# Performance work log

Hardware: AMD Instinct MI355X
Metric: run time of the kernel (lower is better)

The kernel has to match this reference:

```python
import jax, jax.numpy as jnp
import numpy as np
jax.config.update("jax_enable_x64", True)

K = 10            # num_digits
NUM_CLASSES = 10  # digit classes 0..9
EQ_TOKEN = 28
PRIMES = np.array([7, 11, 13, 17, 19, 23, 29, 31, 37], dtype=np.int64)
TWO_PI = 2.0 * np.pi
M_TOTAL = int(np.prod(PRIMES.astype(object)))  # product of primes ~2.47e11 (needs int64)
_crt = []
for p in PRIMES:
    Mi = M_TOTAL // int(p)
    _crt.append((Mi * pow(Mi, -1, int(p))) % M_TOTAL)
CRT_C = jnp.array(_crt, dtype=jnp.int64)                 # [P] CRT mixing coefficients
POW10 = jnp.array([[pow(10, k, int(p)) for k in range(K)] for p in PRIMES], dtype=jnp.float32)  # [P,K]
PR_F = jnp.array(PRIMES, dtype=jnp.float32)
PR_I = jnp.array(PRIMES, dtype=jnp.int64)
POW10_DEC = jnp.array([10 ** k for k in range(K)], dtype=jnp.int64)
_op = np.full(64, -1, dtype=np.int64)
_op[20:25] = np.arange(5)  # tokens 20..24 -> ops add,sub,mul,exp,div
OP_TABLE = jnp.array(_op)


def encode(d):
    # d [B,S,K] soft base-10 digits -> RNS circle encoding [B,S,P,2]
    theta = TWO_PI * jnp.einsum('bsk,pk->bsp', d, POW10) / PR_F
    return jnp.stack([jnp.cos(theta), jnp.sin(theta)], axis=-1)


def decode_residues(circle):
    # [B,S,P,2] -> integer residues mod p, [B,S,P] int64
    theta = jnp.arctan2(circle[..., 1], circle[..., 0])
    r = jnp.round(theta / TWO_PI * PR_F).astype(jnp.int64)
    return jnp.mod(r, PR_I)


def circle_add(a, b):
    ca, sa = a[..., 0], a[..., 1]
    cb, sb = b[..., 0], b[..., 1]
    return jnp.stack([ca * cb - sa * sb, sa * cb + ca * sb], axis=-1)


def circle_sub(a, b):
    ca, sa = a[..., 0], a[..., 1]
    cb, sb = b[..., 0], b[..., 1]
    return jnp.stack([ca * cb + sa * sb, sa * cb - ca * sb], axis=-1)


def modpow(base, exp, mod):
    # elementwise modular exponentiation, exponents < 64 (6 square-and-multiply steps)
    res = jnp.ones_like(base)
    b = jnp.mod(base, mod)
    e = exp
    for _ in range(6):
        res = jnp.where((e & 1) == 1, (res * b) % mod, res)
        b = (b * b) % mod
        e = e >> 1
    return res


def crt(residues):
    # CRT reconstruction: [B,S,P] -> [B,S] int64 in [0, M_TOTAL)
    return jnp.mod(jnp.sum(residues * CRT_C, axis=-1), M_TOTAL)


def crt_signed(residues):
    n = crt(residues)
    return jnp.where(n > M_TOTAL // 2, n - M_TOTAL, n)


def int_to_digits(n):
    # [B,S] int64 -> [B,S,K] float base-10 digits, LSB-first
    return ((n[..., None] // POW10_DEC) % 10).astype(jnp.float32)


def int_to_digits_signed(n):
    sign = (n < 0).astype(jnp.float32)[..., None]
    return jnp.concatenate([int_to_digits(jnp.abs(n)), sign], axis=-1)  # [B,S,K+1]


def decode_all_ops(a_c, b_c):
    # All 5 operations decoded to digit vectors -> [B,S,5K+1]
    ra = decode_residues(a_c)
    rb = decode_residues(b_c)
    add_d = int_to_digits(crt(decode_residues(circle_add(a_c, b_c))))
    sub_d = int_to_digits_signed(crt_signed(decode_residues(circle_sub(a_c, b_c))))
    mul_d = int_to_digits(crt((ra * rb) % PR_I))
    exp_d = int_to_digits(crt(modpow(ra, rb, PR_I)))
    inv = modpow(rb, PR_I - 2, PR_I)  # Fermat inverse
    div_r = jnp.where(rb == 0, 0, (ra * inv) % PR_I)
    div_d = int_to_digits(crt(div_r))
    return jnp.concatenate([add_d, sub_d, mul_d, exp_d, div_d], axis=-1)


def select_op(results, input_ids):
    # [B,S,5K+1] -> [B,S,K+1]: pick the relevant operation per sequence
    B, S, _ = results.shape
    pad = jnp.zeros((B, S, 1), results.dtype)
    ops = jnp.stack([
        jnp.concatenate([results[..., 0:K], pad], -1),
        results[..., K:2 * K + 1],
        jnp.concatenate([results[..., 2 * K + 1:3 * K + 1], pad], -1),
        jnp.concatenate([results[..., 3 * K + 1:4 * K + 1], pad], -1),
        jnp.concatenate([results[..., 4 * K + 1:5 * K + 1], pad], -1),
    ], axis=-2)  # [B,S,5,K+1]
    is_op = OP_TABLE[jnp.clip(input_ids, 0, 63)] >= 0
    op_pos = jnp.argmax(is_op, axis=1)  # first operator position per sequence
    op_tok = jnp.take_along_axis(input_ids, op_pos[:, None], axis=1)[:, 0]
    op_idx = OP_TABLE[jnp.clip(op_tok, 0, 63)]
    gidx = jnp.broadcast_to(jnp.clip(op_idx, 0, 4)[:, None, None, None], (B, S, 1, K + 1))
    sel = jnp.take_along_axis(ops, gidx, axis=-2)[..., 0, :]
    valid = (op_idx >= 0).astype(results.dtype)[:, None, None]
    return sel * valid


def reorder_msb(res):
    # LSB-first digits -> MSB-first, -1 sentinel past the last significant digit
    digits = res[..., :K]
    sign = res[..., K:]
    idx = jnp.arange(K)
    nz = digits != 0
    highest = jnp.max(jnp.where(nz, idx, -1), axis=-1)
    num_sig = jnp.where(jnp.any(nz, axis=-1), highest + 1, 1)
    src = jnp.clip(num_sig[..., None] - 1 - idx, 0, K - 1)
    msb = jnp.take_along_axis(digits, src, axis=-1)
    msb = jnp.where(idx < num_sig[..., None], msb, -1.0)
    return jnp.concatenate([msb, sign], axis=-1)


def setup_inputs() -> dict:
    key = jax.random.key(0)
    ks = jax.random.split(key, 6)
    B, S, D, MH = 16, 2048, 768, 128
    h = jax.random.normal(ks[0], (B, S, D), dtype=jnp.float32)
    input_ids = jax.random.randint(ks[1], (B, S), 0, 50, dtype=jnp.int64)
    W1 = jax.random.normal(ks[2], (D, MH), dtype=jnp.float32) * 0.02
    b1 = jnp.zeros((MH,), jnp.float32)
    W2 = jax.random.normal(ks[3], (MH, 2 * K * NUM_CLASSES), dtype=jnp.float32) * 0.02
    b2 = jnp.zeros((2 * K * NUM_CLASSES,), jnp.float32)
    Winj = jax.random.normal(ks[4], (K + 1, D), dtype=jnp.float32) * 0.001  # injector_init_std
    binj = jnp.zeros((D,), jnp.float32)
    gate_logit = jnp.array(-2.0, jnp.float32)  # gate_init_logit
    return {"h": h, "W1": W1, "b1": b1, "W2": W2, "b2": b2,
            "Winj": Winj, "binj": binj, "gate_logit": gate_logit, "input_ids": input_ids}


def reference(h, W1, b1, W2, b2, Winj, binj, gate_logit, input_ids):
    B, S, D = h.shape
    # OperandExtractor: per-token MLP -> soft digits for operands a and b
    hid = jax.nn.relu(h @ W1 + b1)
    logits = (hid @ W2 + b2).reshape(B, S, 2, K, NUM_CLASSES)
    probs = jax.nn.softmax(logits, axis=-1)
    dig = jnp.einsum('bsokc,c->bsok', probs, jnp.arange(NUM_CLASSES, dtype=h.dtype))
    d_a, d_b = dig[..., 0, :], dig[..., 1, :]
    # RNSCircleEncoder (frozen)
    a_c = encode(d_a)
    b_c = encode(d_b)
    # ArithmeticCompute + CRT decode: detached (torch.no_grad in original)
    results = jax.lax.stop_gradient(decode_all_ops(a_c, b_c).astype(h.dtype))
    sel = select_op(results, input_ids)
    msb = reorder_msb(sel)
    # ResultInjector: gated linear injection into the residual stream
    inj = msb @ Winj + binj
    h_prime = h + jax.nn.sigmoid(gate_logit) * inj
    # only inject for sequences containing the '=' token
    has_eq = jnp.any(input_ids == EQ_TOKEN, axis=1).astype(h.dtype)[:, None, None]
    h_prime = h + (h_prime - h) * has_eq
    return h_prime, d_a, d_b
```

## Files before the change

### kernel.cpp

```cpp
#include <hip/hip_runtime.h>

typedef unsigned short u16;
typedef unsigned int   u32;
typedef unsigned long long u64;
typedef long long i64;

typedef __attribute__((ext_vector_type(8))) short short8;
typedef __attribute__((ext_vector_type(4))) float f32x4;

#define DEV static __device__ __forceinline__

__constant__ float POW10F[9][10] = {
  {1,3,2,6,4,5,1,3,2,6},
  {1,10,1,10,1,10,1,10,1,10},
  {1,10,9,12,3,4,1,10,9,12},
  {1,10,15,14,4,6,9,5,16,7},
  {1,10,5,12,6,3,11,15,17,18},
  {1,10,8,11,18,19,6,14,2,20},
  {1,10,13,14,24,8,22,17,25,18},
  {1,10,7,8,18,25,2,20,14,16},
  {1,10,26,1,10,26,1,10,26,1},
};

#define M_TOTAL  247357937827ull
#define M_HALF   123678968913ull

DEV u16 f2bf_rne(float f){
  u32 u = __float_as_uint(f);
  return (u16)((u + 0x7FFFu + ((u >> 16) & 1u)) >> 16);
}
DEV float bf2f(u16 v){ return __uint_as_float(((u32)v) << 16); }

DEV short8 pack_bf16(float4 a, float4 b){
  union { short8 s; u32 u[4]; } r;
  r.u[0] = (__float_as_uint(a.x) >> 16) | (__float_as_uint(a.y) & 0xFFFF0000u);
  r.u[1] = (__float_as_uint(a.z) >> 16) | (__float_as_uint(a.w) & 0xFFFF0000u);
  r.u[2] = (__float_as_uint(b.x) >> 16) | (__float_as_uint(b.y) & 0xFFFF0000u);
  r.u[3] = (__float_as_uint(b.z) >> 16) | (__float_as_uint(b.w) & 0xFFFF0000u);
  return r.s;
}

DEV void load_lds16(const void* g, void* l){
  __builtin_amdgcn_global_load_lds((const __attribute__((address_space(1))) void*)g,
                                   (__attribute__((address_space(3))) void*)l, 16, 0, 0);
}

DEV int modpow6(int b, int e, int p){
  int res = 1; b %= p;
  #pragma unroll
  for (int i = 0; i < 6; ++i){
    if (e & 1) res = (res * b) % p;
    b = (b * b) % p;
    e >>= 1;
  }
  return res;
}

__global__ void scan_kernel(const int* __restrict__ ids, int* __restrict__ op_idx,
                            float* __restrict__ has_eq){
  __shared__ int smin[256];
  __shared__ int seq[256];
  int b = blockIdx.x, tid = threadIdx.x;
  int best = 2048, eq = 0;
  for (int i = tid; i < 2048; i += 256){
    int t = ids[b * 2048 + i];
    if (t >= 20 && t < 25) best = min(best, i);
    eq |= (t == 28) ? 1 : 0;
  }
  smin[tid] = best; seq[tid] = eq;
  __syncthreads();
  for (int s = 128; s > 0; s >>= 1){
    if (tid < s){ smin[tid] = min(smin[tid], smin[tid + s]); seq[tid] |= seq[tid + s]; }
    __syncthreads();
  }
  if (tid == 0){
    int op = -1;
    if (smin[0] < 2048) op = ids[b * 2048 + smin[0]] - 20;
    op_idx[b] = op;
    has_eq[b] = seq[0] ? 1.0f : 0.0f;
  }
}

__global__ void prep_kernel(const float* __restrict__ W1, const float* __restrict__ W2,
                            u16* __restrict__ w1f, u16* __restrict__ w2f){
  int tid = blockIdx.x * 256 + threadIdx.x;
  if (tid < 12288){
    int blk = tid >> 6, L = tid & 63;
    int T = blk >> 3, b = blk & 7;
    int q = L >> 4, ln = L & 15;
    #pragma unroll
    for (int j = 0; j < 8; ++j){
      int k = 32 * T + 8 * q + j;
      int n = 16 * b + ln;
      w1f[(size_t)blk * 512 + L * 8 + j] = f2bf_rne(W1[k * 128 + n]);
    }
  } else if (tid < 12288 + 3328){
    int t2 = tid - 12288;
    int blk = t2 >> 6, L = t2 & 63;
    int t = blk / 13, b2 = blk % 13;
    int q = L >> 4, ln = L & 15;
    #pragma unroll
    for (int j = 0; j < 8; ++j){
      int k = 32 * t + 8 * q + j;
      int n = 16 * b2 + ln;
      w2f[(size_t)blk * 512 + L * 8 + j] = (n < 200) ? f2bf_rne(W2[k * 200 + n]) : (u16)0;
    }
  }
}

__launch_bounds__(256, 2)
__global__ void pass1_kernel(const float* __restrict__ h, const u16* __restrict__ w1f,
                             const u16* __restrict__ w2f, const float* __restrict__ b1,
                             const float* __restrict__ b2, const int* __restrict__ op_idx_ws,
                             float* __restrict__ dout, u64* __restrict__ msbp){
  __shared__ u16 w1buf[16384];
  __shared__ u16 hidf[4][2048];
  __shared__ float digits_s[64][20];
  __shared__ float tab_s[64][18];
  __shared__ u64 ops_s[64][5];

  const int tid = threadIdx.x;
  const int w = tid >> 6;
  const int lane = tid & 63;
  const int ln = lane & 15, q = lane >> 4;
  const int wg = blockIdx.x;
  const int tok0 = wg * 64;
  const int gtok = tok0 + w * 16 + ln;

  float b1v[8];
  #pragma unroll
  for (int b = 0; b < 8; ++b) b1v[b] = b1[ln + 16 * b];
  float b2v[13];
  #pragma unroll
  for (int b = 0; b < 13; ++b){ int n = ln + 16 * b; b2v[b] = (n < 200) ? b2[n] : 0.0f; }

  f32x4 acc[8];
  #pragma unroll
  for (int b = 0; b < 8; ++b) acc[b] = (f32x4)0.0f;

  const float* hrow = h + (size_t)gtok * 768;
  for (int c = 0; c < 6; ++c){
    float4 xa[4], xb[4];
    const float4* ap = (const float4*)(hrow + c * 128);
    #pragma unroll
    for (int t = 0; t < 4; ++t){
      xa[t] = ap[t * 8 + q * 2];
      xb[t] = ap[t * 8 + q * 2 + 1];
    }
    __syncthreads();
    #pragma unroll
    for (int i = 0; i < 8; ++i){
      int blk = w * 8 + i;
      load_lds16(w1f + (size_t)(c * 32 + blk) * 512 + lane * 8, &w1buf[blk * 512]);
    }
    __syncthreads();
    short8 af[4];
    #pragma unroll
    for (int t = 0; t < 4; ++t) af[t] = pack_bf16(xa[t], xb[t]);
    #pragma unroll
    for (int t = 0; t < 4; ++t){
      #pragma unroll
      for (int b = 0; b < 8; ++b){
        short8 bf = *(const short8*)&w1buf[(t * 8 + b) * 512 + lane * 8];
        acc[b] = __builtin_amdgcn_mfma_f32_16x16x32_bf16(af[t], bf, acc[b], 0, 0, 0);
      }
    }
  }

  #pragma unroll
  for (int b = 0; b < 8; ++b){
    int t2 = b >> 1;
    int q2 = ((b & 1) << 1) | (ln >> 3);
    int j = ln & 7;
    #pragma unroll
    for (int r = 0; r < 4; ++r){
      float v = acc[b][r] + b1v[b];
      v = fmaxf(v, 0.0f);
      int L2 = (q2 << 4) | (q * 4 + r);
      hidf[w][t2 * 512 + L2 * 8 + j] = (u16)(__float_as_uint(v) >> 16);
    }
  }
  __syncthreads();

  short8 a2[4];
  #pragma unroll
  for (int t = 0; t < 4; ++t) a2[t] = *(const short8*)&hidf[w][t * 512 + lane * 8];
  f32x4 acc2[13];
  #pragma unroll
  for (int b = 0; b < 13; ++b) acc2[b] = (f32x4)0.0f;
  #pragma unroll
  for (int b = 0; b < 13; ++b){
    #pragma unroll
    for (int t = 0; t < 4; ++t){
      short8 bf = *(const short8*)(w2f + (size_t)(t * 13 + b) * 512 + lane * 8);
      acc2[b] = __builtin_amdgcn_mfma_f32_16x16x32_bf16(a2[t], bf, acc2[b], 0, 0, 0);
    }
  }

  __syncthreads();

  #pragma unroll
  for (int b = 0; b < 13; ++b){
    #pragma unroll
    for (int r = 0; r < 4; ++r){
      float v = acc2[b][r] + b2v[b];
      w1buf[w * 4096 + (q * 4 + r) * 212 + ln + 16 * b] = (u16)(__float_as_uint(v) >> 16);
    }
  }
  __syncthreads();

  #pragma unroll
  for (int i = 0; i < 5; ++i){
    int task = tid + i * 256;
    int tok = task / 20, slot = task % 20;
    const u16* lp = &w1buf[(tok >> 4) * 4096 + (tok & 15) * 212 + slot * 10];
    float v[10];
    #pragma unroll
    for (int k = 0; k < 10; ++k) v[k] = bf2f(lp[k]);
    float mx = v[0];
    #pragma unroll
    for (int k = 1; k < 10; ++k) mx = fmaxf(mx, v[k]);
    float s = 0.0f, sd = 0.0f;
    #pragma unroll
    for (int k = 0; k < 10; ++k){
      float e = __expf(v[k] - mx);
      s += e; sd += e * (float)k;
    }
    float dig = sd / s;
    digits_s[tok][slot] = dig;
    int gt = tok0 + tok;
    int o = slot / 10, k10 = slot % 10;
    dout[(size_t)25165824 + (size_t)o * 327680 + (size_t)gt * 10 + k10] = dig;
  }
  __syncthreads();

  #pragma unroll
  for (int i = 0; i < 5; ++i){
    int task = tid + i * 256;
    if (task < 1152){
      int tok = task / 18, rm = task % 18;
      int ab = rm / 9, pi = rm % 9;
      float t = 0.0f;
      #pragma unroll
      for (int k = 0; k < 10; ++k) t += digits_s[tok][ab * 10 + k] * POW10F[pi][k];
      tab_s[tok][ab * 9 + pi] = t;
    }
  }
  __syncthreads();

  {
    constexpr int PR[9] = {7, 11, 13, 17, 19, 23, 29, 31, 37};
    constexpr u64 CRTC[9] = {
      35336848261ull, 224870852570ull, 114165202074ull, 218257003965ull,
      78113032998ull, 53773464745ull, 68236672504ull, 223420072876ull, 220616539143ull
    };
    #pragma unroll
    for (int rep = 0; rep < 2; ++rep){
      int task = tid + rep * 256;
      if (task < 320){
        int op = task >> 6, tok = task & 63;
        u64 acc64 = 0;
        #pragma unroll
        for (int pi = 0; pi < 9; ++pi){
          const int p = PR[pi];
          float ta = tab_s[tok][pi], tb = tab_s[tok][9 + pi];
          int r;
          if (op == 0){
            r = __float2int_rn(ta + tb) % p;
          } else if (op == 1){
            int s = __float2int_rn(ta - tb) % p;
            r = (s < 0) ? s + p : s;
          } else {
            int ra = __float2int_rn(ta) % p;
            int rb = __float2int_rn(tb) % p;
            if (op == 2) r = (ra * rb) % p;
            else if (op == 3) r = modpow6(ra, rb, p);
            else r = (rb == 0) ? 0 : (ra * modpow6(rb, p - 2, p)) % p;
          }
          acc64 += (u64)r * CRTC[pi];
        }
        u64 n = acc64 % M_TOTAL;
        int sign = 0;
        u64 un = n;
        if (op == 1 && n > M_HALF){ sign = 1; un = M_TOTAL - n; }
        u64 pk = 0;
        #pragma unroll
        for (int k = 0; k < 10; ++k){ pk |= (un % 10ull) << (4 * k); un /= 10ull; }
        pk |= ((u64)sign) << 40;
        ops_s[tok][op] = pk;
      }
    }
  }
  __syncthreads();

  if (tid < 64){
    int tok = tid;
    int op = op_idx_ws[wg >> 5];
    u64 pk = (op >= 0) ? ops_s[tok][op] : 0ull;
    int g[10]; int hi = -1;
    #pragma unroll
    for (int k = 0; k < 10; ++k){
      g[k] = (int)((pk >> (4 * k)) & 15ull);
      if (g[k] != 0) hi = k;
    }
    int ns = (hi >= 0) ? hi + 1 : 1;
    u64 mp = 0;
    #pragma unroll
    for (int i = 0; i < 10; ++i){
      int v = (i < ns) ? g[ns - 1 - i] : 15;
      mp |= ((u64)v) << (4 * i);
    }
    mp |= ((pk >> 40) & 1ull) << 40;
    msbp[tok0 + tok] = mp;
  }
}

__launch_bounds__(192)
__global__ void pass2_kernel(const float* __restrict__ h, const float* __restrict__ Winj,
                             const float* __restrict__ binj, const float* __restrict__ gate,
                             const float* __restrict__ has_eq_ws,
                             const u64* __restrict__ msbp, float* __restrict__ dout){
  __shared__ u64 smp[16];
  const int tid = threadIdx.x;
  const int tok0 = blockIdx.x * 16;
  if (tid < 16) smp[tid] = msbp[tok0 + tid];

  float4 wv[11];
  #pragma unroll
  for (int j = 0; j < 11; ++j) wv[j] = *(const float4*)(Winj + (size_t)j * 768 + tid * 4);
  float4 bj = *(const float4*)(binj + tid * 4);
  float G = has_eq_ws[tok0 >> 11] * (1.0f / (1.0f + __expf(-gate[0])));
  __syncthreads();

  #pragma unroll 4
  for (int tt = 0; tt < 16; ++tt){
    u64 mp = smp[tt];
    float v[11];
    #pragma unroll
    for (int k = 0; k < 10; ++k){
      int nib = (int)((mp >> (4 * k)) & 15ull);
      v[k] = (nib == 15) ? -1.0f : (float)nib;
    }
    v[10] = (float)((mp >> 40) & 15ull);
    float ix = bj.x, iy = bj.y, iz = bj.z, iw = bj.w;
    #pragma unroll
    for (int j = 0; j < 11; ++j){
      ix += v[j] * wv[j].x; iy += v[j] * wv[j].y;
      iz += v[j] * wv[j].z; iw += v[j] * wv[j].w;
    }
    size_t off = (size_t)(tok0 + tt) * 768 + tid * 4;
    float4 hv = *(const float4*)(h + off);
    float4 o;
    o.x = hv.x + G * ix; o.y = hv.y + G * iy;
    o.z = hv.z + G * iz; o.w = hv.w + G * iw;
    *(float4*)(dout + off) = o;
  }
}

extern "C" void kernel_launch(void* const* d_in, const int* in_sizes, int n_in,
                              void* d_out, int out_size, void* d_ws, size_t ws_size,
                              hipStream_t stream){
  const float* h    = (const float*)d_in[0];
  const float* W1   = (const float*)d_in[1];
  const float* b1   = (const float*)d_in[2];
  const float* W2   = (const float*)d_in[3];
  const float* b2   = (const float*)d_in[4];
  const float* Winj = (const float*)d_in[5];
  const float* binj = (const float*)d_in[6];
  const float* gate = (const float*)d_in[7];
  const int*   ids  = (const int*)d_in[8];
  float* dout = (float*)d_out;

  char* ws = (char*)d_ws;
  int*   op_idx = (int*)(ws + 0);
  float* has_eq = (float*)(ws + 64);
  u16*   w1f    = (u16*)(ws + 256);
  u16*   w2f    = (u16*)(ws + 256 + 196608);
  u64*   msbp   = (u64*)(ws + 250112);

  scan_kernel<<<16, 256, 0, stream>>>(ids, op_idx, has_eq);
  prep_kernel<<<61, 256, 0, stream>>>(W1, W2, w1f, w2f);
  pass1_kernel<<<512, 256, 0, stream>>>(h, w1f, w2f, b1, b2, op_idx, dout, msbp);
  pass2_kernel<<<2048, 192, 0, stream>>>(h, Winj, binj, gate, has_eq, msbp, dout);
}
```

Baseline: 235.1 us.

## Fuse pass1 and pass2 into one kernel, double-buffer W1 tiles, merge prelude kernels

Merges the token scan and weight-prep kernels into one prelude launch. Fuses the MLP/RNS pass with the injection pass, so the MSB digits stay in LDS instead of going through workspace, and the h rows are reread by the same block, likely while still in cache. The W1 GEMM loop now uses half-size LDS tiles with double buffering, prefetching the next tile and the next h slice during the MFMAs. The trade-offs are fewer launches and less global traffic against larger LDS use, the Winj copy into LDS, and only 192 of 256 threads active in the injection phase.

Result: no change. 234.2 us (-0.4%).

```diff
diff --git a/kernel.cpp b/kernel.cpp
--- a/kernel.cpp
+++ b/kernel.cpp
@@ -3,7 +3,6 @@
 typedef unsigned short u16;
 typedef unsigned int   u32;
 typedef unsigned long long u64;
-typedef long long i64;
 
 typedef __attribute__((ext_vector_type(8))) short short8;
 typedef __attribute__((ext_vector_type(4))) float f32x4;
@@ -56,76 +55,89 @@
   return res;
 }
 
-__global__ void scan_kernel(const int* __restrict__ ids, int* __restrict__ op_idx,
-                            float* __restrict__ has_eq){
+__global__ void prelude_kernel(const int* __restrict__ ids, const float* __restrict__ W1,
+                               const float* __restrict__ W2, int* __restrict__ op_idx,
+                               float* __restrict__ has_eq, u16* __restrict__ w1f,
+                               u16* __restrict__ w2f){
   __shared__ int smin[256];
   __shared__ int seq[256];
-  int b = blockIdx.x, tid = threadIdx.x;
-  int best = 2048, eq = 0;
-  for (int i = tid; i < 2048; i += 256){
-    int t = ids[b * 2048 + i];
-    if (t >= 20 && t < 25) best = min(best, i);
-    eq |= (t == 28) ? 1 : 0;
-  }
-  smin[tid] = best; seq[tid] = eq;
-  __syncthreads();
-  for (int s = 128; s > 0; s >>= 1){
-    if (tid < s){ smin[tid] = min(smin[tid], smin[tid + s]); seq[tid] |= seq[tid + s]; }
+  int bid = blockIdx.x, tid = threadIdx.x;
+  if (bid < 16){
+    int b = bid;
+    int best = 2048, eq = 0;
+    for (int i = tid; i < 2048; i += 256){
+      int t = ids[b * 2048 + i];
+      if (t >= 20 && t < 25) best = min(best, i);
+      eq |= (t == 28) ? 1 : 0;
+    }
+    smin[tid] = best; seq[tid] = eq;
     __syncthreads();
-  }
-  if (tid == 0){
-    int op = -1;
-    if (smin[0] < 2048) op = ids[b * 2048 + smin[0]] - 20;
-    op_idx[b] = op;
-    has_eq[b] = seq[0] ? 1.0f : 0.0f;
-  }
-}
-
-__global__ void prep_kernel(const float* __restrict__ W1, const float* __restrict__ W2,
-                            u16* __restrict__ w1f, u16* __restrict__ w2f){
-  int tid = blockIdx.x * 256 + threadIdx.x;
-  if (tid < 12288){
-    int blk = tid >> 6, L = tid & 63;
-    int T = blk >> 3, b = blk & 7;
-    int q = L >> 4, ln = L & 15;
-    #pragma unroll
-    for (int j = 0; j < 8; ++j){
-      int k = 32 * T + 8 * q + j;
-      int n = 16 * b + ln;
-      w1f[(size_t)blk * 512 + L * 8 + j] = f2bf_rne(W1[k * 128 + n]);
-    }
-  } else if (tid < 12288 + 3328){
-    int t2 = tid - 12288;
-    int blk = t2 >> 6, L = t2 & 63;
-    int t = blk / 13, b2 = blk % 13;
-    int q = L >> 4, ln = L & 15;
-    #pragma unroll
-    for (int j = 0; j < 8; ++j){
-      int k = 32 * t + 8 * q + j;
-      int n = 16 * b2 + ln;
-      w2f[(size_t)blk * 512 + L * 8 + j] = (n < 200) ? f2bf_rne(W2[k * 200 + n]) : (u16)0;
+    for (int s = 128; s > 0; s >>= 1){
+      if (tid < s){ smin[tid] = min(smin[tid], smin[tid + s]); seq[tid] |= seq[tid + s]; }
+      __syncthreads();
+    }
+    if (tid == 0){
+      int op = -1;
+      if (smin[0] < 2048) op = ids[b * 2048 + smin[0]] - 20;
+      op_idx[b] = op;
+      has_eq[b] = seq[0] ? 1.0f : 0.0f;
+    }
+  } else {
+    int t = (bid - 16) * 256 + tid;
+    if (t < 12288){
+      int blk = t >> 6, L = t & 63;
+      int T = blk >> 3, b = blk & 7;
+      int q = L >> 4, ln = L & 15;
+      #pragma unroll
+      for (int j = 0; j < 8; ++j){
+        int k = 32 * T + 8 * q + j;
+        int n = 16 * b + ln;
+        w1f[(size_t)blk * 512 + L * 8 + j] = f2bf_rne(W1[k * 128 + n]);
+      }
+    } else {
+      int t2 = t - 12288;
+      int blk = t2 >> 6, L = t2 & 63;
+      int ts = blk / 13, b2 = blk % 13;
+      int q = L >> 4, ln = L & 15;
+      #pragma unroll
+      for (int j = 0; j < 8; ++j){
+        int k = 32 * ts + 8 * q + j;
+        int n = 16 * b2 + ln;
+        w2f[(size_t)blk * 512 + L * 8 + j] = (n < 200) ? f2bf_rne(W2[k * 200 + n]) : (u16)0;
+      }
     }
   }
 }
 
 __launch_bounds__(256, 2)
-__global__ void pass1_kernel(const float* __restrict__ h, const u16* __restrict__ w1f,
-                             const u16* __restrict__ w2f, const float* __restrict__ b1,
-                             const float* __restrict__ b2, const int* __restrict__ op_idx_ws,
-                             float* __restrict__ dout, u64* __restrict__ msbp){
-  __shared__ u16 w1buf[16384];
-  __shared__ u16 hidf[4][2048];
-  __shared__ float digits_s[64][20];
-  __shared__ float tab_s[64][18];
-  __shared__ u64 ops_s[64][5];
-
-  const int tid = threadIdx.x;
-  const int w = tid >> 6;
+__global__ void mega_kernel(const float* __restrict__ h, const u16* __restrict__ w1f,
+                            const u16* __restrict__ w2f, const float* __restrict__ b1,
+                            const float* __restrict__ b2, const float* __restrict__ Winj,
+                            const float* __restrict__ binj, const float* __restrict__ gate,
+                            const int* __restrict__ op_idx_ws, const float* __restrict__ has_eq_ws,
+                            float* __restrict__ dout){
+  __shared__ __align__(16) char lds[49152];
+  u16*   wbuf     = (u16*)lds;
+  char*  tail     = lds + 32768;
+  float* digits_s = (float*)tail;
+  float* tab_s    = (float*)(tail + 5120);
+  u64*   ops_s    = (u64*)(tail + 9728);
+  float* msbv     = (float*)(tail + 12288);
+  u16*   hidf     = (u16*)tail;
+  float* winj_s   = (float*)lds;
+  float* binj_s   = (float*)(lds + 33792);
+
+  const int tid  = threadIdx.x;
+  const int w    = tid >> 6;
   const int lane = tid & 63;
-  const int ln = lane & 15, q = lane >> 4;
-  const int wg = blockIdx.x;
+  const int ln   = lane & 15, q = lane >> 4;
+  const int wg   = blockIdx.x;
   const int tok0 = wg * 64;
   const int gtok = tok0 + w * 16 + ln;
+  const int batch = wg >> 5;
+
+  const int   op = op_idx_ws[batch];
+  const float G  = has_eq_ws[batch] * (1.0f / (1.0f + __expf(-gate[0])));
 
   float b1v[8];
   #pragma unroll
@@ -138,30 +150,43 @@
   #pragma unroll
   for (int b = 0; b < 8; ++b) acc[b] = (f32x4)0.0f;
 
-  const float* hrow = h + (size_t)gtok * 768;
-  for (int c = 0; c < 6; ++c){
-    float4 xa[4], xb[4];
-    const float4* ap = (const float4*)(hrow + c * 128);
-    #pragma unroll
-    for (int t = 0; t < 4; ++t){
-      xa[t] = ap[t * 8 + q * 2];
-      xb[t] = ap[t * 8 + q * 2 + 1];
-    }
+  const float4* ap = (const float4*)(h + (size_t)gtok * 768);
+  float4 xa[2], xb[2];
+  #pragma unroll
+  for (int i = 0; i < 4; ++i){
+    int bl = w * 4 + i;
+    load_lds16(w1f + (size_t)(((bl >> 3)) * 8 + (bl & 7)) * 512 + lane * 8,
+               wbuf + bl * 512);
+  }
+  #pragma unroll
+  for (int t = 0; t < 2; ++t){ xa[t] = ap[t * 8 + q * 2]; xb[t] = ap[t * 8 + q * 2 + 1]; }
+
+  #pragma unroll
+  for (int c = 0; c < 12; ++c){
     __syncthreads();
-    #pragma unroll
-    for (int i = 0; i < 8; ++i){
-      int blk = w * 8 + i;
-      load_lds16(w1f + (size_t)(c * 32 + blk) * 512 + lane * 8, &w1buf[blk * 512]);
-    }
-    __syncthreads();
-    short8 af[4];
-    #pragma unroll
-    for (int t = 0; t < 4; ++t) af[t] = pack_bf16(xa[t], xb[t]);
-    #pragma unroll
-    for (int t = 0; t < 4; ++t){
+    const u16* cur = wbuf + (c & 1) * 8192;
+    if (c < 11){
+      u16* nxt = wbuf + ((c + 1) & 1) * 8192;
+      #pragma unroll
+      for (int i = 0; i < 4; ++i){
+        int bl = w * 4 + i;
+        int T  = (c + 1) * 2 + (bl >> 3);
+        load_lds16(w1f + (size_t)(T * 8 + (bl & 7)) * 512 + lane * 8, nxt + bl * 512);
+      }
+    }
+    short8 af[2];
+    #pragma unroll
+    for (int t = 0; t < 2; ++t) af[t] = pack_bf16(xa[t], xb[t]);
+    if (c < 11){
+      const float4* ap2 = ap + (c + 1) * 16;
+      #pragma unroll
+      for (int t = 0; t < 2; ++t){ xa[t] = ap2[t * 8 + q * 2]; xb[t] = ap2[t * 8 + q * 2 + 1]; }
+    }
+    #pragma unroll
+    for (int t = 0; t < 2; ++t){
       #pragma unroll
       for (int b = 0; b < 8; ++b){
-        short8 bf = *(const short8*)&w1buf[(t * 8 + b) * 512 + lane * 8];
+        short8 bf = *(const short8*)(cur + (t * 8 + b) * 512 + lane * 8);
         acc[b] = __builtin_amdgcn_mfma_f32_16x16x32_bf16(af[t], bf, acc[b], 0, 0, 0);
       }
     }
@@ -171,20 +196,19 @@
   for (int b = 0; b < 8; ++b){
     int t2 = b >> 1;
     int q2 = ((b & 1) << 1) | (ln >> 3);
-    int j = ln & 7;
+    int j  = ln & 7;
     #pragma unroll
     for (int r = 0; r < 4; ++r){
-      float v = acc[b][r] + b1v[b];
-      v = fmaxf(v, 0.0f);
+      float v = fmaxf(acc[b][r] + b1v[b], 0.0f);
       int L2 = (q2 << 4) | (q * 4 + r);
-      hidf[w][t2 * 512 + L2 * 8 + j] = (u16)(__float_as_uint(v) >> 16);
+      hidf[w * 2048 + t2 * 512 + L2 * 8 + j] = (u16)(__float_as_uint(v) >> 16);
     }
   }
   __syncthreads();
 
   short8 a2[4];
   #pragma unroll
-  for (int t = 0; t < 4; ++t) a2[t] = *(const short8*)&hidf[w][t * 512 + lane * 8];
+  for (int t = 0; t < 4; ++t) a2[t] = *(const short8*)(hidf + w * 2048 + t * 512 + lane * 8);
   f32x4 acc2[13];
   #pragma unroll
   for (int b = 0; b < 13; ++b) acc2[b] = (f32x4)0.0f;
@@ -197,14 +221,12 @@
     }
   }
 
-  __syncthreads();
-
   #pragma unroll
   for (int b = 0; b < 13; ++b){
     #pragma unroll
     for (int r = 0; r < 4; ++r){
       float v = acc2[b][r] + b2v[b];
-      w1buf[w * 4096 + (q * 4 + r) * 212 + ln + 16 * b] = (u16)(__float_as_uint(v) >> 16);
+      wbuf[w * 4096 + (q * 4 + r) * 212 + ln + 16 * b] = (u16)(__float_as_uint(v) >> 16);
     }
   }
   __syncthreads();
@@ -213,7 +235,7 @@
   for (int i = 0; i < 5; ++i){
     int task = tid + i * 256;
     int tok = task / 20, slot = task % 20;
-    const u16* lp = &w1buf[(tok >> 4) * 4096 + (tok & 15) * 212 + slot * 10];
+    const u16* lp = wbuf + (tok >> 4) * 4096 + (tok & 15) * 212 + slot * 10;
     float v[10];
     #pragma unroll
     for (int k = 0; k < 10; ++k) v[k] = bf2f(lp[k]);
@@ -227,12 +249,19 @@
       s += e; sd += e * (float)k;
     }
     float dig = sd / s;
-    digits_s[tok][slot] = dig;
+    digits_s[tok * 20 + slot] = dig;
     int gt = tok0 + tok;
     int o = slot / 10, k10 = slot % 10;
     dout[(size_t)25165824 + (size_t)o * 327680 + (size_t)gt * 10 + k10] = dig;
   }
   __syncthreads();
+
+  #pragma unroll
+  for (int i = 0; i < 8; ++i){
+    int idx = tid + i * 256;
+    float4 vsrc = *(const float4*)(Winj + (size_t)idx * 4);
+    *(float4*)(winj_s + (size_t)idx * 4) = vsrc;
+  }
 
   #pragma unroll
   for (int i = 0; i < 5; ++i){
@@ -242,11 +271,27 @@
       int ab = rm / 9, pi = rm % 9;
       float t = 0.0f;
       #pragma unroll
-      for (int k = 0; k < 10; ++k) t += digits_s[tok][ab * 10 + k] * POW10F[pi][k];
-      tab_s[tok][ab * 9 + pi] = t;
-    }
-  }
-  __syncthreads();
+      for (int k = 0; k < 10; ++k) t += digits_s[tok * 20 + ab * 10 + k] * POW10F[pi][k];
+      tab_s[tok * 18 + ab * 9 + pi] = t;
+    }
+  }
+  __syncthreads();
+
+  {
+    int idx = 2048 + (tid >> 1) + ((tid & 1) ? 224 : 0);
+  }
+  if (tid < 224){
+    #pragma unroll
+    for (int i = 0; i < 2; ++i){
+      int idx = 2048 + tid + i * 224;
+      if (idx < 2496){
+        const float* src = (idx < 2112) ? (Winj + (size_t)idx * 4)
+                                        : (binj + (size_t)(idx - 2112) * 4);
+        float4 vsrc = *(const float4*)src;
+        *(float4*)(winj_s + (size_t)idx * 4) = vsrc;
+      }
+    }
+  }
 
   {
     constexpr int PR[9] = {7, 11, 13, 17, 19, 23, 29, 31, 37};
@@ -258,23 +303,23 @@
     for (int rep = 0; rep < 2; ++rep){
       int task = tid + rep * 256;
       if (task < 320){
-        int op = task >> 6, tok = task & 63;
+        int o5 = task >> 6, tok = task & 63;
         u64 acc64 = 0;
         #pragma unroll
         for (int pi = 0; pi < 9; ++pi){
           const int p = PR[pi];
-          float ta = tab_s[tok][pi], tb = tab_s[tok][9 + pi];
+          float ta = tab_s[tok * 18 + pi], tb = tab_s[tok * 18 + 9 + pi];
           int r;
-          if (op == 0){
+          if (o5 == 0){
             r = __float2int_rn(ta + tb) % p;
-          } else if (op == 1){
+          } else if (o5 == 1){
             int s = __float2int_rn(ta - tb) % p;
             r = (s < 0) ? s + p : s;
           } else {
             int ra = __float2int_rn(ta) % p;
             int rb = __float2int_rn(tb) % p;
-            if (op == 2) r = (ra * rb) % p;
-            else if (op == 3) r = modpow6(ra, rb, p);
+            if (o5 == 2) r = (ra * rb) % p;
+            else if (o5 == 3) r = modpow6(ra, rb, p);
             else r = (rb == 0) ? 0 : (ra * modpow6(rb, p - 2, p)) % p;
           }
           acc64 += (u64)r * CRTC[pi];
@@ -282,12 +327,12 @@
         u64 n = acc64 % M_TOTAL;
         int sign = 0;
         u64 un = n;
-        if (op == 1 && n > M_HALF){ sign = 1; un = M_TOTAL - n; }
+        if (o5 == 1 && n > M_HALF){ sign = 1; un = M_TOTAL - n; }
         u64 pk = 0;
         #pragma unroll
         for (int k = 0; k < 10; ++k){ pk |= (un % 10ull) << (4 * k); un /= 10ull; }
         pk |= ((u64)sign) << 40;
-        ops_s[tok][op] = pk;
+        ops_s[tok * 5 + o5] = pk;
       }
     }
   }
@@ -295,8 +340,7 @@
 
   if (tid < 64){
     int tok = tid;
-    int op = op_idx_ws[wg >> 5];
-    u64 pk = (op >= 0) ? ops_s[tok][op] : 0ull;
+    u64 pk = (op >= 0) ? ops_s[tok * 5 + op] : 0ull;
     int g[10]; int hi = -1;
     #pragma unroll
     for (int k = 0; k < 10; ++k){
@@ -304,56 +348,44 @@
       if (g[k] != 0) hi = k;
     }
     int ns = (hi >= 0) ? hi + 1 : 1;
-    u64 mp = 0;
-    #pragma unroll
-    for (int i = 0; i < 10; ++i){
-      int v = (i < ns) ? g[ns - 1 - i] : 15;
-      mp |= ((u64)v) << (4 * i);
-    }
-    mp |= ((pk >> 40) & 1ull) << 40;
-    msbp[tok0 + tok] = mp;
-  }
-}
-
-__launch_bounds__(192)
-__global__ void pass2_kernel(const float* __restrict__ h, const float* __restrict__ Winj,
-                             const float* __restrict__ binj, const float* __restrict__ gate,
-                             const float* __restrict__ has_eq_ws,
-                             const u64* __restrict__ msbp, float* __restrict__ dout){
-  __shared__ u64 smp[16];
-  const int tid = threadIdx.x;
-  const int tok0 = blockIdx.x * 16;
-  if (tid < 16) smp[tid] = msbp[tok0 + tid];
-
-  float4 wv[11];
-  #pragma unroll
-  for (int j = 0; j < 11; ++j) wv[j] = *(const float4*)(Winj + (size_t)j * 768 + tid * 4);
-  float4 bj = *(const float4*)(binj + tid * 4);
-  float G = has_eq_ws[tok0 >> 11] * (1.0f / (1.0f + __expf(-gate[0])));
-  __syncthreads();
-
-  #pragma unroll 4
-  for (int tt = 0; tt < 16; ++tt){
-    u64 mp = smp[tt];
-    float v[11];
-    #pragma unroll
-    for (int k = 0; k < 10; ++k){
-      int nib = (int)((mp >> (4 * k)) & 15ull);
-      v[k] = (nib == 15) ? -1.0f : (float)nib;
-    }
-    v[10] = (float)((mp >> 40) & 15ull);
-    float ix = bj.x, iy = bj.y, iz = bj.z, iw = bj.w;
-    #pragma unroll
-    for (int j = 0; j < 11; ++j){
-      ix += v[j] * wv[j].x; iy += v[j] * wv[j].y;
-      iz += v[j] * wv[j].z; iw += v[j] * wv[j].w;
-    }
-    size_t off = (size_t)(tok0 + tt) * 768 + tid * 4;
-    float4 hv = *(const float4*)(h + off);
-    float4 o;
-    o.x = hv.x + G * ix; o.y = hv.y + G * iy;
-    o.z = hv.z + G * iz; o.w = hv.w + G * iw;
-    *(float4*)(dout + off) = o;
+    #pragma unroll
+    for (int i = 0; i < 10; ++i)
+      msbv[tok * 12 + i] = (i < ns) ? (float)g[ns - 1 - i] : -1.0f;
+    msbv[tok * 12 + 10] = (float)((pk >> 40) & 1ull);
+    msbv[tok * 12 + 11] = 0.0f;
+  }
+  __syncthreads();
+
+  if (tid < 192){
+    float4 wv[11];
+    #pragma unroll
+    for (int j = 0; j < 11; ++j) wv[j] = *(const float4*)(winj_s + j * 768 + tid * 4);
+    float4 bj = *(const float4*)(binj_s + tid * 4);
+    const size_t base = (size_t)tok0 * 768 + tid * 4;
+    #pragma unroll 4
+    for (int tt = 0; tt < 64; ++tt){
+      float4 m0 = *(const float4*)(msbv + tt * 12);
+      float4 m1 = *(const float4*)(msbv + tt * 12 + 4);
+      float4 m2 = *(const float4*)(msbv + tt * 12 + 8);
+      float4 hv = *(const float4*)(h + base + (size_t)tt * 768);
+      float ix = bj.x, iy = bj.y, iz = bj.z, iw = bj.w;
+      ix += m0.x*wv[0].x + m0.y*wv[1].x + m0.z*wv[2].x + m0.w*wv[3].x
+          + m1.x*wv[4].x + m1.y*wv[5].x + m1.z*wv[6].x + m1.w*wv[7].x
+          + m2.x*wv[8].x + m2.y*wv[9].x + m2.z*wv[10].x;
+      iy += m0.x*wv[0].y + m0.y*wv[1].y + m0.z*wv[2].y + m0.w*wv[3].y
+          + m1.x*wv[4].y + m1.y*wv[5].y + m1.z*wv[6].y + m1.w*wv[7].y
+          + m2.x*wv[8].y + m2.y*wv[9].y + m2.z*wv[10].y;
+      iz += m0.x*wv[0].z + m0.y*wv[1].z + m0.z*wv[2].z + m0.w*wv[3].z
+          + m1.x*wv[4].z + m1.y*wv[5].z + m1.z*wv[6].z + m1.w*wv[7].z
+          + m2.x*wv[8].z + m2.y*wv[9].z + m2.z*wv[10].z;
+      iw += m0.x*wv[0].w + m0.y*wv[1].w + m0.z*wv[2].w + m0.w*wv[3].w
+          + m1.x*wv[4].w + m1.y*wv[5].w + m1.z*wv[6].w + m1.w*wv[7].w
+          + m2.x*wv[8].w + m2.y*wv[9].w + m2.z*wv[10].w;
+      float4 o;
+      o.x = hv.x + G * ix; o.y = hv.y + G * iy;
+      o.z = hv.z + G * iz; o.w = hv.w + G * iw;
+      *(float4*)(dout + base + (size_t)tt * 768) = o;
+    }
   }
 }
 
@@ -376,10 +408,8 @@
   float* has_eq = (float*)(ws + 64);
   u16*   w1f    = (u16*)(ws + 256);
   u16*   w2f    = (u16*)(ws + 256 + 196608);
-  u64*   msbp   = (u64*)(ws + 250112);
-
-  scan_kernel<<<16, 256, 0, stream>>>(ids, op_idx, has_eq);
-  prep_kernel<<<61, 256, 0, stream>>>(W1, W2, w1f, w2f);
-  pass1_kernel<<<512, 256, 0, stream>>>(h, w1f, w2f, b1, b2, op_idx, dout, msbp);
-  pass2_kernel<<<2048, 192, 0, stream>>>(h, Winj, binj, gate, has_eq, msbp, dout);
-}
+
+  prelude_kernel<<<77, 256, 0, stream>>>(ids, W1, W2, op_idx, has_eq, w1f, w2f);
+  mega_kernel<<<512, 256, 0, stream>>>(h, w1f, w2f, b1, b2, Winj, binj, gate,
+                                       op_idx, has_eq, dout);
+}
```
